# Optimization experiments

Measured on AMD Instinct MI355X. Metric: run time of the kernel, lower is better.

Reference implementation:

```python
import jax, jax.numpy as jnp
import numpy as np

B, S = 128, 512
VOCAB, E, H, T = 100000, 100, 128, 10  # tagset_size=10 -> CRF over T-1=9 tags
HD = H // 2  # per-direction LSTM hidden


def setup_inputs():
    key = jax.random.key(0)
    ks = jax.random.split(key, 14)
    s = 0.08
    inputs = jax.random.randint(ks[0], (B, S), 1, VOCAB)
    tags = jax.random.randint(ks[1], (B, S), 1, T)  # valid after tags-1 shift
    mask = jnp.ones((B, S), dtype=bool)
    emb = (jax.random.normal(ks[2], (VOCAB, E)) * s).at[0].set(0.0)  # padding_idx=0 row zeroed
    Wih_f = jax.random.normal(ks[3], (4 * HD, E)) * s
    Whh_f = jax.random.normal(ks[4], (4 * HD, HD)) * s
    b_f = jax.random.normal(ks[5], (4 * HD,)) * s
    Wih_b = jax.random.normal(ks[6], (4 * HD, E)) * s
    Whh_b = jax.random.normal(ks[7], (4 * HD, HD)) * s
    b_b = jax.random.normal(ks[8], (4 * HD,)) * s
    W_out = jax.random.normal(ks[9], (T, H)) * s
    b_out = jax.random.normal(ks[10], (T,)) * s
    start = jax.random.normal(ks[11], (T - 1,)) * s
    end = jax.random.normal(ks[12], (T - 1,)) * s
    trans = jax.random.normal(ks[13], (T - 1, T - 1)) * s
    return dict(inputs=inputs, tags=tags, mask=mask, emb=emb,
                Wih_f=Wih_f, Whh_f=Whh_f, b_f=b_f,
                Wih_b=Wih_b, Whh_b=Whh_b, b_b=b_b,
                W_out=W_out, b_out=b_out, start=start, end=end, trans=trans)


def _lstm_dir(x, Wih, Whh, b, reverse):
    # x: [S, B, E] time-major; PyTorch gate order i,f,g,o; b = b_ih + b_hh
    h0 = jnp.zeros((x.shape[1], Whh.shape[1]), x.dtype)

    def step(carry, xt):
        h, c = carry
        gates = xt @ Wih.T + h @ Whh.T + b
        i, f, g, o = jnp.split(gates, 4, axis=-1)
        c = jax.nn.sigmoid(f) * c + jax.nn.sigmoid(i) * jnp.tanh(g)
        h = jax.nn.sigmoid(o) * jnp.tanh(c)
        return (h, c), h

    _, hs = jax.lax.scan(step, (h0, h0), x, reverse=reverse)
    return hs  # [S, B, HD]


def _crf_nll(em, tags, mask, start, end, trans):
    # Linear-chain CRF (torchcrf-style). em: [S,B,K], tags/mask: [S,B]
    pick = lambda e, t: jnp.take_along_axis(e, t[:, None], axis=-1)[:, 0]
    # numerator: score of the gold path
    score0 = start[tags[0]] + pick(em[0], tags[0])

    def num_step(sc, inp):
        em_t, t, tp, m = inp
        return sc + jnp.where(m, trans[tp, t] + pick(em_t, t), 0.0), None

    score, _ = jax.lax.scan(num_step, score0, (em[1:], tags[1:], tags[:-1], mask[1:]))
    last_idx = mask.sum(0).astype(jnp.int32) - 1
    last_tags = jnp.take_along_axis(tags, last_idx[None, :], axis=0)[0]
    score = score + end[last_tags]
    # denominator: forward algorithm (log partition)
    alpha0 = start[None, :] + em[0]  # [B,K]

    def fwd_step(alpha, inp):
        em_t, m = inp
        nxt = jax.nn.logsumexp(alpha[:, :, None] + trans[None, :, :] + em_t[:, None, :], axis=1)
        return jnp.where(m[:, None], nxt, alpha), None

    alpha, _ = jax.lax.scan(fwd_step, alpha0, (em[1:], mask[1:]))
    logZ = jax.nn.logsumexp(alpha + end[None, :], axis=1)
    return -(score - logZ).mean()  # loss = -log_likelihood.mean()


def _forward(inputs, tags, mask, emb, Wih_f, Whh_f, b_f, Wih_b, Whh_b, b_b, W_out, b_out, start, end, trans):
    x = emb[inputs].transpose(1, 0, 2)  # [S,B,E]
    h = jnp.concatenate([_lstm_dir(x, Wih_f, Whh_f, b_f, False),
                         _lstm_dir(x, Wih_b, Whh_b, b_b, True)], axis=-1)  # [S,B,H]
    # dropout is identity at eval; slice off tag 0 as in the module
    em = (h @ W_out.T + b_out)[:, :, 1:]  # [S,B,T-1]
    return _crf_nll(em, (tags - 1).T, mask.T, start, end, trans)


def reference(inputs, tags, mask, emb, Wih_f, Whh_f, b_f, Wih_b, Whh_b, b_b, W_out, b_out, start, end, trans):
    return _forward(inputs, tags, mask, emb, Wih_f, Whh_f, b_f, Wih_b, Whh_b, b_b, W_out, b_out, start, end, trans)
```

## Files before the change

### kernel.cpp

```cpp
#include <hip/hip_runtime.h>
#include <math.h>

#define SB 512
#define NB 128
#define HD 64

typedef _Float16 h2 __attribute__((ext_vector_type(2)));
typedef _Float16 f16x8 __attribute__((ext_vector_type(8)));
typedef float f32x4 __attribute__((ext_vector_type(4)));
union U4 { uint4 u; h2 h[4]; _Float16 f[8]; };
union UF { uint4 u; f16x8 h8; _Float16 f[8]; };
union U2 { uint2 u; _Float16 f[4]; };
union UH { unsigned u; _Float16 f[2]; };

__device__ __forceinline__ float frcp(float x) { return __builtin_amdgcn_rcpf(x); }
__device__ __forceinline__ float fsig(float x) { return frcp(1.0f + __expf(-x)); }
__device__ __forceinline__ float ftanh(float x) {
    float t = __expf(-2.0f * fabsf(x));
    float r = (1.0f - t) * frcp(1.0f + t);
    return copysignf(r, x);
}
__device__ __forceinline__ float fdot2(h2 a, h2 b, float c) {
    return __builtin_amdgcn_fdot2(a, b, c, false);
}

__global__ __launch_bounds__(256, 2) void gemm_kernel(
    const int* __restrict__ inputs, const float* __restrict__ emb,
    const float* __restrict__ Wih_f, const float* __restrict__ Wih_bb,
    const float* __restrict__ b_f, const float* __restrict__ b_bb,
    _Float16* __restrict__ xgh)
{
    __shared__ __align__(16) unsigned sE[128 * 68];
    __shared__ __align__(16) unsigned sW[128 * 68];
    __shared__ float sbias[512];
    __shared__ int stok[128];
    const int tt = blockIdx.x;
    const int tid = threadIdx.x;
    const int w = tid >> 6, l = tid & 63;
    const int q = l >> 4, n = l & 15;

    if (tid < 128) stok[tid] = inputs[tid * SB + tt];
    for (int i = tid; i < 512; i += 256) {
        int dir = i >> 8, r = i & 255, jj = r >> 2, g = r & 3;
        sbias[i] = (dir ? b_bb : b_f)[g * 64 + jj];
    }
    __syncthreads();
    for (int idx = tid; idx < 8192; idx += 256) {
        int row = idx >> 6, d = idx & 63;
        unsigned v = 0;
        if (d < 50) {
            const float* ep = emb + (size_t)stok[row] * 100 + 2 * d;
            UH u; u.f[0] = (_Float16)ep[0]; u.f[1] = (_Float16)ep[1];
            v = u.u;
        }
        sE[row * 68 + d] = v;
    }

    for (int cg = 0; cg < 4; ++cg) {
        __syncthreads();
        for (int idx = tid; idx < 2048; idx += 256) {
            int col = cg * 128 + (idx >> 4);
            int dir = col >> 8, r = col & 255, jj = r >> 2, g = r & 3;
            const float* base = (dir ? Wih_bb : Wih_f) + (g * 64 + jj) * 100;
            int dq = idx & 15;
            UF pack; pack.u = make_uint4(0, 0, 0, 0);
            if (dq < 12) {
                float4 f0 = *(const float4*)(base + 8 * dq);
                float4 f1 = *(const float4*)(base + 8 * dq + 4);
                pack.f[0] = (_Float16)f0.x; pack.f[1] = (_Float16)f0.y;
                pack.f[2] = (_Float16)f0.z; pack.f[3] = (_Float16)f0.w;
                pack.f[4] = (_Float16)f1.x; pack.f[5] = (_Float16)f1.y;
                pack.f[6] = (_Float16)f1.z; pack.f[7] = (_Float16)f1.w;
            } else if (dq == 12) {
                float4 f0 = *(const float4*)(base + 96);
                pack.f[0] = (_Float16)f0.x; pack.f[1] = (_Float16)f0.y;
                pack.f[2] = (_Float16)f0.z; pack.f[3] = (_Float16)f0.w;
            }
            ((uint4*)sW)[(idx >> 4) * 17 + dq] = pack.u;
        }
        __syncthreads();

        f32x4 acc[2][8];
        #pragma unroll
        for (int m = 0; m < 2; ++m)
            #pragma unroll
            for (int c = 0; c < 8; ++c)
                #pragma unroll
                for (int r = 0; r < 4; ++r) acc[m][c][r] = 0.f;

        #pragma unroll
        for (int kt = 0; kt < 4; ++kt) {
            const int ko = 16 * kt + 2 * q;
            UF A0, A1;
            {
                const unsigned* rp = &sE[(16 * (2 * w + 0) + n) * 68 + ko];
                uint2 lo = *(const uint2*)rp;
                uint2 hi = *(const uint2*)(rp + 8);
                A0.u = make_uint4(lo.x, lo.y, hi.x, hi.y);
                rp = &sE[(16 * (2 * w + 1) + n) * 68 + ko];
                lo = *(const uint2*)rp;
                hi = *(const uint2*)(rp + 8);
                A1.u = make_uint4(lo.x, lo.y, hi.x, hi.y);
            }
            UF B[8];
            #pragma unroll
            for (int c = 0; c < 8; ++c) {
                const unsigned* rp = &sW[(16 * c + n) * 68 + ko];
                uint2 lo = *(const uint2*)rp;
                uint2 hi = *(const uint2*)(rp + 8);
                B[c].u = make_uint4(lo.x, lo.y, hi.x, hi.y);
            }
            #pragma unroll
            for (int c = 0; c < 8; ++c) {
                acc[0][c] = __builtin_amdgcn_mfma_f32_16x16x32_f16(A0.h8, B[c].h8, acc[0][c], 0, 0, 0);
                acc[1][c] = __builtin_amdgcn_mfma_f32_16x16x32_f16(A1.h8, B[c].h8, acc[1][c], 0, 0, 0);
            }
        }

        #pragma unroll
        for (int m = 0; m < 2; ++m)
            #pragma unroll
            for (int c = 0; c < 8; ++c) {
                int col = cg * 128 + 16 * c + n;
                float bc = sbias[col];
                #pragma unroll
                for (int r = 0; r < 4; ++r) {
                    int row = 16 * (2 * w + m) + 4 * q + r;
                    xgh[(size_t)(tt * NB + row) * 512 + col] = (_Float16)(acc[m][c][r] + bc);
                }
            }
    }
}

__global__ __attribute__((amdgpu_flat_work_group_size(64, 64), amdgpu_waves_per_eu(1, 1)))
void lstm_kernel(
    const _Float16* __restrict__ xgh, const float* __restrict__ Whh_f,
    const float* __restrict__ Whh_bb, _Float16* __restrict__ h16)
{
    const int blk = blockIdx.x;
    const int b = blk & (NB - 1);
    const int dir = blk >> 7;
    const int j = threadIdx.x;

    __shared__ __align__(16) unsigned wlds[8192];
    __shared__ __align__(16) _Float16 hbuf[64];

    {
        const float* Wsrc = dir ? Whh_bb : Whh_f;
        uint4* dst = (uint4*)wlds;
        #pragma unroll
        for (int i = 0; i < 32; ++i) {
            int g = i >> 3, k4 = i & 7;
            const float* rp = Wsrc + (g * 64 + j) * 64 + 8 * k4;
            float4 f0 = *(const float4*)rp;
            float4 f1 = *(const float4*)(rp + 4);
            UF pack;
            pack.f[0] = (_Float16)f0.x; pack.f[1] = (_Float16)f0.y;
            pack.f[2] = (_Float16)f0.z; pack.f[3] = (_Float16)f0.w;
            pack.f[4] = (_Float16)f1.x; pack.f[5] = (_Float16)f1.y;
            pack.f[6] = (_Float16)f1.z; pack.f[7] = (_Float16)f1.w;
            dst[i * 64 + j] = pack.u;
        }
    }
    hbuf[j] = (_Float16)0.f;
    float c = 0.f;

    const int t0 = dir ? (SB - 1) : 0;
    const ptrdiff_t xstride = (dir ? -1 : 1) * (ptrdiff_t)(NB * 512);
    const _Float16* xp = xgh + ((size_t)(t0 * NB + b)) * 512 + dir * 256 + j * 4;
    _Float16* hp = h16 + ((size_t)(b * 2 + dir) * SB + t0) * 64 + j;
    const ptrdiff_t hstride = (dir ? -1 : 1) * (ptrdiff_t)64;

    U2 p0, p1, p2;
    p0.u = *(const uint2*)xp;
    p1.u = *(const uint2*)(xp + xstride);
    p2.u = *(const uint2*)(xp + 2 * xstride);
    const _Float16* xq = xp + 3 * xstride;

    const uint4* wl = (const uint4*)wlds;

    for (int s = 0; s < SB; ++s) {
        float a0 = (float)p0.f[0], a1 = (float)p0.f[1];
        float a2 = (float)p0.f[2], a3 = (float)p0.f[3];
        p0 = p1; p1 = p2;
        p2.u = *(const uint2*)xq;
        xq += xstride;

        U4 hv[8];
        #pragma unroll
        for (int k4 = 0; k4 < 8; ++k4) hv[k4].u = *(const uint4*)&hbuf[k4 * 8];

        float g0[4] = {a0, 0.f, 0.f, 0.f};
        float g1[4] = {a1, 0.f, 0.f, 0.f};
        float g2[4] = {a2, 0.f, 0.f, 0.f};
        float g3[4] = {a3, 0.f, 0.f, 0.f};
        #pragma unroll
        for (int k4 = 0; k4 < 8; ++k4) {
            U4 w0, w1, w2, w3;
            w0.u = wl[(0 * 8 + k4) * 64 + j];
            w1.u = wl[(1 * 8 + k4) * 64 + j];
            w2.u = wl[(2 * 8 + k4) * 64 + j];
            w3.u = wl[(3 * 8 + k4) * 64 + j];
            const int p = k4 & 3;
            #pragma unroll
            for (int q = 0; q < 4; ++q) {
                g0[p] = fdot2(hv[k4].h[q], w0.h[q], g0[p]);
                g1[p] = fdot2(hv[k4].h[q], w1.h[q], g1[p]);
                g2[p] = fdot2(hv[k4].h[q], w2.h[q], g2[p]);
                g3[p] = fdot2(hv[k4].h[q], w3.h[q], g3[p]);
            }
        }
        a0 = (g0[0] + g0[1]) + (g0[2] + g0[3]);
        a1 = (g1[0] + g1[1]) + (g1[2] + g1[3]);
        a2 = (g2[0] + g2[1]) + (g2[2] + g2[3]);
        a3 = (g3[0] + g3[1]) + (g3[2] + g3[3]);

        float ig = fsig(a0), fg = fsig(a1), gg = ftanh(a2), og = fsig(a3);
        c = fg * c + ig * gg;
        float h = og * ftanh(c);
        *hp = (_Float16)h;
        hp += hstride;
        hbuf[j] = (_Float16)h;
    }
}

__global__ __launch_bounds__(256, 1) void pgs_kernel(
    const _Float16* __restrict__ h16, const float* __restrict__ W_out,
    const float* __restrict__ b_out, const int* __restrict__ tags,
    const float* __restrict__ startv, const float* __restrict__ endv,
    const float* __restrict__ trans, float* __restrict__ parts)
{
    __shared__ __align__(16) unsigned tile[128 * 64];
    __shared__ __align__(16) float em3L[SB * 12];
    __shared__ __align__(16) unsigned sWo[9 * 64];
    __shared__ float sb[9];
    __shared__ float sEexp[81];
    __shared__ float sgold;
    const int b = blockIdx.x, tid = threadIdx.x;
    float* Pst = (float*)tile;

    for (int i2 = tid; i2 < 576; i2 += 256) {
        int k = i2 >> 6, jp = i2 & 63;
        const float* src = W_out + (k + 1) * 128 + 2 * jp;
        UH u; u.f[0] = (_Float16)src[0]; u.f[1] = (_Float16)src[1];
        sWo[i2] = u.u;
    }
    if (tid < 9) sb[tid] = b_out[1 + tid];
    if (tid < 81) sEexp[tid] = __expf(trans[tid]);

    for (int tt = 0; tt < 4; ++tt) {
        const int t0 = tt * 128;
        __syncthreads();
        #pragma unroll
        for (int dir = 0; dir < 2; ++dir) {
            const unsigned* src = (const unsigned*)(h16 + ((size_t)(b * 2 + dir) * SB + t0) * 64);
            for (int i = tid; i < 4096; i += 256) {
                int t = i >> 5, jp = i & 31;
                tile[t * 64 + dir * 32 + jp] = src[i];
            }
        }
        __syncthreads();

        for (int o = tid; o < 1152; o += 256) {
            int tl = o / 9, k = o - 9 * tl;
            const U4* hr = (const U4*)&tile[tl * 64];
            const U4* wr = (const U4*)&sWo[k * 64];
            float pa = 0.f, pb = 0.f;
            #pragma unroll
            for (int qq = 0; qq < 16; qq += 2) {
                U4 hv = hr[qq], wv = wr[qq];
                U4 hv2 = hr[qq + 1], wv2 = wr[qq + 1];
                #pragma unroll
                for (int z = 0; z < 4; ++z) {
                    pa = fdot2(hv.h[z], wv.h[z], pa);
                    pb = fdot2(hv2.h[z], wv2.h[z], pb);
                }
            }
            em3L[(t0 + tl) * 12 + k] = pa + pb + sb[k];
        }
    }
    __syncthreads();

    if (tid >= 64 && tid < 128) {
        const int l = tid - 64;
        const int* tb = tags + (size_t)b * SB;
        float sc = 0.f;
        for (int t = l; t < SB; t += 64) {
            int tg = tb[t] - 1;
            if (t > 0) {
                int tp = tb[t - 1] - 1;
                sc += trans[tp * 9 + tg] + em3L[t * 12 + tg];
            }
        }
        if (l == 0) {
            int tg0 = tb[0] - 1, tgl = tb[SB - 1] - 1;
            sc += startv[tg0] + em3L[tg0] + endv[tgl];
        }
        #pragma unroll
        for (int off = 32; off > 0; off >>= 1) sc += __shfl_down(sc, off);
        if (l == 0) sgold = sc;
    }

    if (tid < 32) {
        const int c = tid;
        float E[81];
        #pragma unroll
        for (int i = 0; i < 81; ++i) E[i] = sEexp[i];

        float P[81];
        #pragma unroll
        for (int i = 0; i < 81; ++i) P[i] = 0.f;
        #pragma unroll
        for (int i = 0; i < 9; ++i) P[i * 9 + i] = 1.f;
        float M = 0.f;

        const int t0 = 1 + 16 * c;
        const int nst = (t0 + 16 <= SB) ? 16 : (SB - t0);
        const float* ep = &em3L[t0 * 12];

        for (int s = 0; s < nst; ++s, ep += 12) {
            float4 e0 = *(const float4*)ep;
            float4 e1 = *(const float4*)(ep + 4);
            float e8 = ep[8];
            float ex[9] = { __expf(e0.x), __expf(e0.y), __expf(e0.z), __expf(e0.w),
                            __expf(e1.x), __expf(e1.y), __expf(e1.z), __expf(e1.w),
                            __expf(e8) };
            #pragma unroll
            for (int i = 0; i < 9; ++i) {
                float tmp[9];
                #pragma unroll
                for (int jj = 0; jj < 9; ++jj) tmp[jj] = P[i * 9] * E[jj];
                #pragma unroll
                for (int k = 1; k < 9; ++k)
                    #pragma unroll
                    for (int jj = 0; jj < 9; ++jj) tmp[jj] += P[i * 9 + k] * E[k * 9 + jj];
                #pragma unroll
                for (int jj = 0; jj < 9; ++jj) P[i * 9 + jj] = tmp[jj] * ex[jj];
            }
            if ((s & 3) == 3) {
                float mx = P[0];
                #pragma unroll
                for (int i = 1; i < 81; ++i) mx = fmaxf(mx, P[i]);
                M += __logf(mx);
                float r = frcp(mx);
                #pragma unroll
                for (int i = 0; i < 81; ++i) P[i] *= r;
            }
        }

        float* dst = &Pst[c * 84];
        #pragma unroll
        for (int i = 0; i < 81; ++i) dst[i] = P[i];
        dst[81] = M;
    }
    __syncthreads();

    if (tid < 64) {
        float A[9], M = 0.f;
        #pragma unroll
        for (int k = 0; k < 9; ++k) A[k] = __expf(startv[k] + em3L[k]);

        for (int c = 0; c < 32; ++c) {
            const float4* src = (const float4*)&Pst[c * 84];
            float buf[84];
            #pragma unroll
            for (int qq = 0; qq < 21; ++qq) {
                float4 v = src[qq];
                buf[4 * qq] = v.x; buf[4 * qq + 1] = v.y; buf[4 * qq + 2] = v.z; buf[4 * qq + 3] = v.w;
            }
            float tmp[9];
            #pragma unroll
            for (int jj = 0; jj < 9; ++jj) tmp[jj] = A[0] * buf[jj];
            #pragma unroll
            for (int i = 1; i < 9; ++i)
                #pragma unroll
                for (int jj = 0; jj < 9; ++jj) tmp[jj] += A[i] * buf[i * 9 + jj];
            float mx = tmp[0];
            #pragma unroll
            for (int jj = 1; jj < 9; ++jj) mx = fmaxf(mx, tmp[jj]);
            M += __logf(mx) + buf[81];
            float r = frcp(mx);
            #pragma unroll
            for (int jj = 0; jj < 9; ++jj) A[jj] = tmp[jj] * r;
        }

        float Z = 0.f;
        #pragma unroll
        for (int k = 0; k < 9; ++k) Z += A[k] * __expf(endv[k]);
        float part = M + __logf(Z) - sgold;
        if (tid == 0) parts[b] = part;
    }
}

__global__ __launch_bounds__(128, 1) void crf_combine2(
    const float* __restrict__ parts, float* __restrict__ out)
{
    const int b = threadIdx.x;
    float part = parts[b];
    #pragma unroll
    for (int off = 32; off > 0; off >>= 1) part += __shfl_down(part, off);
    __shared__ float sm[2];
    if ((b & 63) == 0) sm[b >> 6] = part;
    __syncthreads();
    if (b == 0) out[0] = (sm[0] + sm[1]) * (1.0f / NB);
}

extern "C" void kernel_launch(void* const* d_in, const int* in_sizes, int n_in,
                              void* d_out, int out_size, void* d_ws, size_t ws_size,
                              hipStream_t stream)
{
    const int*   inputs = (const int*)d_in[0];
    const int*   tags   = (const int*)d_in[1];
    const float* emb    = (const float*)d_in[3];
    const float* Wih_f  = (const float*)d_in[4];
    const float* Whh_f  = (const float*)d_in[5];
    const float* b_f    = (const float*)d_in[6];
    const float* Wih_b  = (const float*)d_in[7];
    const float* Whh_b  = (const float*)d_in[8];
    const float* b_b    = (const float*)d_in[9];
    const float* W_out  = (const float*)d_in[10];
    const float* b_out  = (const float*)d_in[11];
    const float* startv = (const float*)d_in[12];
    const float* endv   = (const float*)d_in[13];
    const float* transv = (const float*)d_in[14];

    char* w = (char*)d_ws;
    float* parts   = (float*)w;     w += (size_t)NB * SB * 12 * 4;
    _Float16* xgh  = (_Float16*)w;  w += (size_t)SB * NB * 512 * 2;
    _Float16* h16  = (_Float16*)w;  w += (size_t)NB * 2 * SB * 64 * 2;
    (void)w;

    gemm_kernel<<<SB, 256, 0, stream>>>(inputs, emb, Wih_f, Wih_b, b_f, b_b, xgh);
    lstm_kernel<<<256, 64, 0, stream>>>(xgh, Whh_f, Whh_b, h16);
    pgs_kernel<<<NB, 256, 0, stream>>>(h16, W_out, b_out, tags, startv, endv, transv, parts);
    crf_combine2<<<1, 128, 0, stream>>>(parts, (float*)d_out);
}
```

Measured before the change: 452.7 us.

## Fuse LSTM, CRF partition and final reduction into one per-sequence kernel

Merges the LSTM recurrence, the emission/CRF kernel and the final mean reduction into a single kernel with one block per batch element. Both directions of the LSTM run in the same block on two waves, with LDS shared with the CRF stage. The last-finishing block, found through an atomic counter, does the final sum. This removes two kernel launches and the intermediate launch gaps. The trade-off is that the LSTM now runs in 128 blocks of 256 threads instead of 256 single-wave blocks, so occupancy drops and the two directions share one CU.

```diff
diff --git a/kernel.cpp b/kernel.cpp
--- a/kernel.cpp
+++ b/kernel.cpp
@@ -28,7 +28,7 @@
     const int* __restrict__ inputs, const float* __restrict__ emb,
     const float* __restrict__ Wih_f, const float* __restrict__ Wih_bb,
     const float* __restrict__ b_f, const float* __restrict__ b_bb,
-    _Float16* __restrict__ xgh)
+    _Float16* __restrict__ xgh, unsigned* __restrict__ cnt)
 {
     __shared__ __align__(16) unsigned sE[128 * 68];
     __shared__ __align__(16) unsigned sW[128 * 68];
@@ -38,6 +38,8 @@
     const int tid = threadIdx.x;
     const int w = tid >> 6, l = tid & 63;
     const int q = l >> 4, n = l & 15;
+
+    if (tt == 0 && tid == 0) *cnt = 0u;
 
     if (tid < 128) stok[tid] = inputs[tid * SB + tt];
     for (int i = tid; i < 512; i += 256) {
@@ -132,121 +134,122 @@
     }
 }
 
-__global__ __attribute__((amdgpu_flat_work_group_size(64, 64), amdgpu_waves_per_eu(1, 1)))
-void lstm_kernel(
+__global__ __launch_bounds__(256, 1) void mega_kernel(
     const _Float16* __restrict__ xgh, const float* __restrict__ Whh_f,
-    const float* __restrict__ Whh_bb, _Float16* __restrict__ h16)
+    const float* __restrict__ Whh_bb, _Float16* __restrict__ h16,
+    const float* __restrict__ W_out, const float* __restrict__ b_out,
+    const int* __restrict__ tags, const float* __restrict__ startv,
+    const float* __restrict__ endv, const float* __restrict__ trans,
+    float* __restrict__ parts, unsigned* __restrict__ cnt,
+    float* __restrict__ out)
 {
-    const int blk = blockIdx.x;
-    const int b = blk & (NB - 1);
-    const int dir = blk >> 7;
-    const int j = threadIdx.x;
-
-    __shared__ __align__(16) unsigned wlds[8192];
-    __shared__ __align__(16) _Float16 hbuf[64];
-
-    {
-        const float* Wsrc = dir ? Whh_bb : Whh_f;
-        uint4* dst = (uint4*)wlds;
-        #pragma unroll
-        for (int i = 0; i < 32; ++i) {
-            int g = i >> 3, k4 = i & 7;
-            const float* rp = Wsrc + (g * 64 + j) * 64 + 8 * k4;
-            float4 f0 = *(const float4*)rp;
-            float4 f1 = *(const float4*)(rp + 4);
-            UF pack;
-            pack.f[0] = (_Float16)f0.x; pack.f[1] = (_Float16)f0.y;
-            pack.f[2] = (_Float16)f0.z; pack.f[3] = (_Float16)f0.w;
-            pack.f[4] = (_Float16)f1.x; pack.f[5] = (_Float16)f1.y;
-            pack.f[6] = (_Float16)f1.z; pack.f[7] = (_Float16)f1.w;
-            dst[i * 64 + j] = pack.u;
-        }
-    }
-    hbuf[j] = (_Float16)0.f;
-    float c = 0.f;
-
-    const int t0 = dir ? (SB - 1) : 0;
-    const ptrdiff_t xstride = (dir ? -1 : 1) * (ptrdiff_t)(NB * 512);
-    const _Float16* xp = xgh + ((size_t)(t0 * NB + b)) * 512 + dir * 256 + j * 4;
-    _Float16* hp = h16 + ((size_t)(b * 2 + dir) * SB + t0) * 64 + j;
-    const ptrdiff_t hstride = (dir ? -1 : 1) * (ptrdiff_t)64;
-
-    U2 p0, p1, p2;
-    p0.u = *(const uint2*)xp;
-    p1.u = *(const uint2*)(xp + xstride);
-    p2.u = *(const uint2*)(xp + 2 * xstride);
-    const _Float16* xq = xp + 3 * xstride;
-
-    const uint4* wl = (const uint4*)wlds;
-
-    for (int s = 0; s < SB; ++s) {
-        float a0 = (float)p0.f[0], a1 = (float)p0.f[1];
-        float a2 = (float)p0.f[2], a3 = (float)p0.f[3];
-        p0 = p1; p1 = p2;
-        p2.u = *(const uint2*)xq;
-        xq += xstride;
-
-        U4 hv[8];
-        #pragma unroll
-        for (int k4 = 0; k4 < 8; ++k4) hv[k4].u = *(const uint4*)&hbuf[k4 * 8];
-
-        float g0[4] = {a0, 0.f, 0.f, 0.f};
-        float g1[4] = {a1, 0.f, 0.f, 0.f};
-        float g2[4] = {a2, 0.f, 0.f, 0.f};
-        float g3[4] = {a3, 0.f, 0.f, 0.f};
-        #pragma unroll
-        for (int k4 = 0; k4 < 8; ++k4) {
-            U4 w0, w1, w2, w3;
-            w0.u = wl[(0 * 8 + k4) * 64 + j];
-            w1.u = wl[(1 * 8 + k4) * 64 + j];
-            w2.u = wl[(2 * 8 + k4) * 64 + j];
-            w3.u = wl[(3 * 8 + k4) * 64 + j];
-            const int p = k4 & 3;
-            #pragma unroll
-            for (int q = 0; q < 4; ++q) {
-                g0[p] = fdot2(hv[k4].h[q], w0.h[q], g0[p]);
-                g1[p] = fdot2(hv[k4].h[q], w1.h[q], g1[p]);
-                g2[p] = fdot2(hv[k4].h[q], w2.h[q], g2[p]);
-                g3[p] = fdot2(hv[k4].h[q], w3.h[q], g3[p]);
-            }
-        }
-        a0 = (g0[0] + g0[1]) + (g0[2] + g0[3]);
-        a1 = (g1[0] + g1[1]) + (g1[2] + g1[3]);
-        a2 = (g2[0] + g2[1]) + (g2[2] + g2[3]);
-        a3 = (g3[0] + g3[1]) + (g3[2] + g3[3]);
-
-        float ig = fsig(a0), fg = fsig(a1), gg = ftanh(a2), og = fsig(a3);
-        c = fg * c + ig * gg;
-        float h = og * ftanh(c);
-        *hp = (_Float16)h;
-        hp += hstride;
-        hbuf[j] = (_Float16)h;
-    }
-}
-
-__global__ __launch_bounds__(256, 1) void pgs_kernel(
-    const _Float16* __restrict__ h16, const float* __restrict__ W_out,
-    const float* __restrict__ b_out, const int* __restrict__ tags,
-    const float* __restrict__ startv, const float* __restrict__ endv,
-    const float* __restrict__ trans, float* __restrict__ parts)
-{
-    __shared__ __align__(16) unsigned tile[128 * 64];
+    __shared__ __align__(16) unsigned uni[16384];
     __shared__ __align__(16) float em3L[SB * 12];
     __shared__ __align__(16) unsigned sWo[9 * 64];
     __shared__ float sb[9];
     __shared__ float sEexp[81];
+    __shared__ __align__(16) _Float16 hbuf2[2][64];
     __shared__ float sgold;
+    __shared__ int sflag;
+    __shared__ float sm2[2];
     const int b = blockIdx.x, tid = threadIdx.x;
-    float* Pst = (float*)tile;
-
-    for (int i2 = tid; i2 < 576; i2 += 256) {
-        int k = i2 >> 6, jp = i2 & 63;
-        const float* src = W_out + (k + 1) * 128 + 2 * jp;
-        UH u; u.f[0] = (_Float16)src[0]; u.f[1] = (_Float16)src[1];
-        sWo[i2] = u.u;
-    }
-    if (tid < 9) sb[tid] = b_out[1 + tid];
-    if (tid < 81) sEexp[tid] = __expf(trans[tid]);
+
+    if (tid < 128) {
+        const int dir = tid >> 6;
+        const int j = tid & 63;
+        unsigned* wlds = &uni[dir * 8192];
+        {
+            const float* Wsrc = dir ? Whh_bb : Whh_f;
+            uint4* dst = (uint4*)wlds;
+            #pragma unroll
+            for (int i = 0; i < 32; ++i) {
+                int g = i >> 3, k4 = i & 7;
+                const float* rp = Wsrc + (g * 64 + j) * 64 + 8 * k4;
+                float4 f0 = *(const float4*)rp;
+                float4 f1 = *(const float4*)(rp + 4);
+                UF pack;
+                pack.f[0] = (_Float16)f0.x; pack.f[1] = (_Float16)f0.y;
+                pack.f[2] = (_Float16)f0.z; pack.f[3] = (_Float16)f0.w;
+                pack.f[4] = (_Float16)f1.x; pack.f[5] = (_Float16)f1.y;
+                pack.f[6] = (_Float16)f1.z; pack.f[7] = (_Float16)f1.w;
+                dst[i * 64 + j] = pack.u;
+            }
+        }
+        hbuf2[dir][j] = (_Float16)0.f;
+        float c = 0.f;
+
+        const int t0 = dir ? (SB - 1) : 0;
+        const ptrdiff_t xstride = (dir ? -1 : 1) * (ptrdiff_t)(NB * 512);
+        const _Float16* xp = xgh + ((size_t)(t0 * NB + b)) * 512 + dir * 256 + j * 4;
+        _Float16* hp = h16 + ((size_t)(b * 2 + dir) * SB + t0) * 64 + j;
+        const ptrdiff_t hstride = (dir ? -1 : 1) * (ptrdiff_t)64;
+
+        U2 p0, p1, p2;
+        p0.u = *(const uint2*)xp;
+        p1.u = *(const uint2*)(xp + xstride);
+        p2.u = *(const uint2*)(xp + 2 * xstride);
+        const _Float16* xq = xp + 3 * xstride;
+
+        const uint4* wl = (const uint4*)wlds;
+        _Float16* hb = &hbuf2[dir][0];
+
+        for (int s = 0; s < SB; ++s) {
+            float a0 = (float)p0.f[0], a1 = (float)p0.f[1];
+            float a2 = (float)p0.f[2], a3 = (float)p0.f[3];
+            p0 = p1; p1 = p2;
+            p2.u = *(const uint2*)xq;
+            xq += xstride;
+
+            U4 hv[8];
+            #pragma unroll
+            for (int k4 = 0; k4 < 8; ++k4) hv[k4].u = *(const uint4*)&hb[k4 * 8];
+
+            float g0[4] = {a0, 0.f, 0.f, 0.f};
+            float g1[4] = {a1, 0.f, 0.f, 0.f};
+            float g2[4] = {a2, 0.f, 0.f, 0.f};
+            float g3[4] = {a3, 0.f, 0.f, 0.f};
+            #pragma unroll
+            for (int k4 = 0; k4 < 8; ++k4) {
+                U4 w0, w1, w2, w3;
+                w0.u = wl[(0 * 8 + k4) * 64 + j];
+                w1.u = wl[(1 * 8 + k4) * 64 + j];
+                w2.u = wl[(2 * 8 + k4) * 64 + j];
+                w3.u = wl[(3 * 8 + k4) * 64 + j];
+                const int p = k4 & 3;
+                #pragma unroll
+                for (int q = 0; q < 4; ++q) {
+                    g0[p] = fdot2(hv[k4].h[q], w0.h[q], g0[p]);
+                    g1[p] = fdot2(hv[k4].h[q], w1.h[q], g1[p]);
+                    g2[p] = fdot2(hv[k4].h[q], w2.h[q], g2[p]);
+                    g3[p] = fdot2(hv[k4].h[q], w3.h[q], g3[p]);
+                }
+            }
+            a0 = (g0[0] + g0[1]) + (g0[2] + g0[3]);
+            a1 = (g1[0] + g1[1]) + (g1[2] + g1[3]);
+            a2 = (g2[0] + g2[1]) + (g2[2] + g2[3]);
+            a3 = (g3[0] + g3[1]) + (g3[2] + g3[3]);
+
+            float ig = fsig(a0), fg = fsig(a1), gg = ftanh(a2), og = fsig(a3);
+            c = fg * c + ig * gg;
+            float h = og * ftanh(c);
+            *hp = (_Float16)h;
+            hp += hstride;
+            hb[j] = (_Float16)h;
+        }
+    } else {
+        for (int i2 = tid - 128; i2 < 576; i2 += 128) {
+            int k = i2 >> 6, jp = i2 & 63;
+            const float* src = W_out + (k + 1) * 128 + 2 * jp;
+            UH u; u.f[0] = (_Float16)src[0]; u.f[1] = (_Float16)src[1];
+            sWo[i2] = u.u;
+        }
+        if (tid - 128 < 9) sb[tid - 128] = b_out[1 + tid - 128];
+        if (tid - 128 < 81) sEexp[tid - 128] = __expf(trans[tid - 128]);
+    }
+    __syncthreads();
+
+    unsigned* tile = uni;
+    float* Pst = (float*)uni;
 
     for (int tt = 0; tt < 4; ++tt) {
         const int t0 = tt * 128;
@@ -355,6 +358,7 @@
     }
     __syncthreads();
 
+    float part = 0.f;
     if (tid < 64) {
         float A[9], M = 0.f;
         #pragma unroll
@@ -387,22 +391,28 @@
         float Z = 0.f;
         #pragma unroll
         for (int k = 0; k < 9; ++k) Z += A[k] * __expf(endv[k]);
-        float part = M + __logf(Z) - sgold;
-        if (tid == 0) parts[b] = part;
-    }
-}
-
-__global__ __launch_bounds__(128, 1) void crf_combine2(
-    const float* __restrict__ parts, float* __restrict__ out)
-{
-    const int b = threadIdx.x;
-    float part = parts[b];
-    #pragma unroll
-    for (int off = 32; off > 0; off >>= 1) part += __shfl_down(part, off);
-    __shared__ float sm[2];
-    if ((b & 63) == 0) sm[b >> 6] = part;
+        part = M + __logf(Z) - sgold;
+    }
+
+    if (tid == 0) {
+        atomicExch(&parts[b], part);
+        __threadfence();
+        unsigned old = atomicAdd(cnt, 1u);
+        sflag = (old == NB - 1) ? 1 : 0;
+    }
     __syncthreads();
-    if (b == 0) out[0] = (sm[0] + sm[1]) * (1.0f / NB);
+    if (sflag) {
+        float v = 0.f;
+        if (tid < NB) v = atomicAdd(&parts[tid], 0.0f);
+        #pragma unroll
+        for (int off = 32; off > 0; off >>= 1) v += __shfl_down(v, off);
+        if (tid < NB && (tid & 63) == 0) sm2[tid >> 6] = v;
+        __syncthreads();
+        if (tid == 0) {
+            out[0] = (sm2[0] + sm2[1]) * (1.0f / NB);
+            atomicExch(cnt, 0u);
+        }
+    }
 }
 
 extern "C" void kernel_launch(void* const* d_in, const int* in_sizes, int n_in,
@@ -425,13 +435,14 @@
     const float* transv = (const float*)d_in[14];
 
     char* w = (char*)d_ws;
-    float* parts   = (float*)w;     w += (size_t)NB * SB * 12 * 4;
+    float* parts   = (float*)w;
+    unsigned* cnt  = (unsigned*)(w + NB * 4);
+    w += (size_t)NB * SB * 12 * 4;
     _Float16* xgh  = (_Float16*)w;  w += (size_t)SB * NB * 512 * 2;
     _Float16* h16  = (_Float16*)w;  w += (size_t)NB * 2 * SB * 64 * 2;
     (void)w;
 
-    gemm_kernel<<<SB, 256, 0, stream>>>(inputs, emb, Wih_f, Wih_b, b_f, b_b, xgh);
-    lstm_kernel<<<256, 64, 0, stream>>>(xgh, Whh_f, Whh_b, h16);
-    pgs_kernel<<<NB, 256, 0, stream>>>(h16, W_out, b_out, tags, startv, endv, transv, parts);
-    crf_combine2<<<1, 128, 0, stream>>>(parts, (float*)d_out);
+    gemm_kernel<<<SB, 256, 0, stream>>>(inputs, emb, Wih_f, Wih_b, b_f, b_b, xgh, cnt);
+    mega_kernel<<<NB, 256, 0, stream>>>(xgh, Whh_f, Whh_b, h16, W_out, b_out, tags,
+                                        startv, endv, transv, parts, cnt, (float*)d_out);
 }
```

Result: no change. 449.7 us (-0.7%).
